# Kernel tuning notes

Hardware: AMD Instinct MI355X
Metric: run time of the kernel (lower is better)

## Reference

```python
import jax, jax.numpy as jnp
import numpy as np

N, E, DIN, H, OUT = 100000, 1600000, 64, 128, 2
BN_EPS = 1e-5


def _mlp_bn(h, wa, ba, g, be, wb, bb):
    # PyG MLP([d_in, H, H]): lin -> batch_norm (train-mode batch stats) -> relu -> lin (plain last)
    h = h @ wa + ba
    mu = jnp.mean(h, axis=0)
    var = jnp.mean((h - mu) ** 2, axis=0)  # biased var, as in BatchNorm training
    h = g * (h - mu) * jax.lax.rsqrt(var + BN_EPS) + be
    h = jax.nn.relu(h)
    return h @ wb + bb


def _gin_layer(x, src, dst, wa, ba, g, be, wb, bb, eps):
    # sum-aggregate neighbor features: agg[i] = sum_{(j->i) in E} x[j]
    agg = jax.ops.segment_sum(x[src], dst, num_segments=N)
    h = (1.0 + eps) * x + agg
    h = _mlp_bn(h, wa, ba, g, be, wb, bb)
    return jax.nn.relu(h)  # GIN.forward outer activation (dropout p=0)


def setup_inputs() -> dict:
    key = jax.random.key(0)
    ks = iter(jax.random.split(key, 40))
    d = {}
    d['x'] = jax.random.normal(next(ks), (N, DIN), dtype=jnp.float32)
    d['edge_index'] = jax.random.randint(next(ks), (2, E), 0, N, dtype=jnp.int64)

    def lin(k, fi, fo):
        return jax.random.normal(k, (fi, fo), dtype=jnp.float32) * (1.0 / np.sqrt(fi))

    fin = DIN
    for l in range(3):
        d[f'w{l}a'] = lin(next(ks), fin, H)
        d[f'b{l}a'] = jnp.zeros((H,), jnp.float32)
        d[f'g{l}'] = jnp.ones((H,), jnp.float32)
        d[f'be{l}'] = jnp.zeros((H,), jnp.float32)
        d[f'w{l}b'] = lin(next(ks), H, H)
        d[f'b{l}b'] = jnp.zeros((H,), jnp.float32)
        d[f'eps{l}'] = jnp.zeros((), jnp.float32)
        fin = H
    d['hwa'] = lin(next(ks), H, H)
    d['hba'] = jnp.zeros((H,), jnp.float32)
    d['hwb'] = lin(next(ks), H, OUT)
    d['hbb'] = jnp.zeros((OUT,), jnp.float32)
    return d


def reference(x, edge_index,
              w0a, b0a, g0, be0, w0b, b0b, eps0,
              w1a, b1a, g1, be1, w1b, b1b, eps1,
              w2a, b2a, g2, be2, w2b, b2b, eps2,
              hwa, hba, hwb, hbb):
    src, dst = edge_index[0], edge_index[1]
    h = _gin_layer(x, src, dst, w0a, b0a, g0, be0, w0b, b0b, eps0)
    h = _gin_layer(h, src, dst, w1a, b1a, g1, be1, w1b, b1b, eps1)
    h = _gin_layer(h, src, dst, w2a, b2a, g2, be2, w2b, b2b, eps2)
    # head MLP([H, H, OUT], norm=None, dropout=0): lin -> relu -> lin
    h = jax.nn.relu(h @ hwa + hba)
    return h @ hwb + hbb
```

## Files before the change

kernel.cpp:

```cpp
#include <hip/hip_runtime.h>

#define NN 100000
#define NE 1600000
#define HD 128
#define NB1 391
#define GG  782

typedef unsigned short u16;
typedef __attribute__((ext_vector_type(8))) short bf16x8;
typedef __attribute__((ext_vector_type(4))) float f32x4;

__device__ __forceinline__ u16 f2b(float f) {
    unsigned u = __builtin_bit_cast(unsigned, f);
    unsigned r = (u + 0x7FFFu + ((u >> 16) & 1u)) >> 16;
    return (u16)r;
}
__device__ __forceinline__ float b2f(u16 h) {
    unsigned u = ((unsigned)h) << 16;
    return __builtin_bit_cast(float, u);
}
__device__ __forceinline__ float lof(unsigned v) {
    return __builtin_bit_cast(float, v << 16);
}
__device__ __forceinline__ float hif(unsigned v) {
    return __builtin_bit_cast(float, v & 0xFFFF0000u);
}
__device__ __forceinline__ unsigned pack2(float a, float b) {
    return (unsigned)f2b(a) | ((unsigned)f2b(b) << 16);
}

__global__ __launch_bounds__(256)
void k_hist(const int* __restrict__ dst, int* __restrict__ degree,
            int* __restrict__ off) {
    int e = blockIdx.x * 256 + threadIdx.x;
    if (e < NE) off[e] = atomicAdd(degree + dst[e], 1);
}

__global__ __launch_bounds__(256)
void k_scan_blk(const int* __restrict__ degree, int* __restrict__ incl,
                int* __restrict__ bsum) {
    __shared__ int s[256];
    int t = threadIdx.x;
    int i = blockIdx.x * 256 + t;
    int v = (i < NN) ? degree[i] : 0;
    s[t] = v;
    __syncthreads();
    #pragma unroll
    for (int off = 1; off < 256; off <<= 1) {
        int tmp = (t >= off) ? s[t - off] : 0;
        __syncthreads();
        s[t] += tmp;
        __syncthreads();
    }
    if (i < NN) incl[i] = s[t];
    if (t == 255) bsum[blockIdx.x] = s[255];
}

__global__ __launch_bounds__(512)
void k_scan_top(const int* __restrict__ bsum, int* __restrict__ bscan) {
    __shared__ int s[512];
    int t = threadIdx.x;
    s[t] = (t < NB1) ? bsum[t] : 0;
    __syncthreads();
    #pragma unroll
    for (int off = 1; off < 512; off <<= 1) {
        int tmp = (t >= off) ? s[t - off] : 0;
        __syncthreads();
        s[t] += tmp;
        __syncthreads();
    }
    if (t < NB1) bscan[t] = s[t];
}

__global__ __launch_bounds__(256)
void k_scan_fix(const int* __restrict__ incl, const int* __restrict__ bscan,
                int* __restrict__ rowptr) {
    int i = blockIdx.x * 256 + threadIdx.x;
    if (i < NN) {
        int off = (blockIdx.x > 0) ? bscan[blockIdx.x - 1] : 0;
        rowptr[i + 1] = incl[i] + off;
        if (i == 0) rowptr[0] = 0;
    }
}

__global__ __launch_bounds__(256)
void k_scatter(const int* __restrict__ src, const int* __restrict__ dst,
               const int* __restrict__ rowptr, const int* __restrict__ off,
               int* __restrict__ eidx) {
    int e = blockIdx.x * 256 + threadIdx.x;
    if (e < NE) {
        eidx[rowptr[dst[e]] + off[e]] = src[e];
    }
}

__global__ __launch_bounds__(256)
void k_cvt(const float* __restrict__ in, u16* __restrict__ out, int n4) {
    for (int i = blockIdx.x * 256 + threadIdx.x; i < n4; i += gridDim.x * 256) {
        float4 v = reinterpret_cast<const float4*>(in)[i];
        uint2 o;
        o.x = pack2(v.x, v.y);
        o.y = pack2(v.z, v.w);
        *reinterpret_cast<uint2*>(out + (size_t)i * 4) = o;
    }
}

template<int F>
__global__ __launch_bounds__(64)
void k_aggr(const u16* __restrict__ x, const int* __restrict__ rowptr,
            const int* __restrict__ eidx, const float* __restrict__ epsp,
            u16* __restrict__ out) {
    const int n = blockIdx.x;
    const int t = threadIdx.x;
    const int p0 = rowptr[n], p1 = rowptr[n + 1];
    const float e1 = 1.0f + epsp[0];

    if constexpr (F == 128) {
        const unsigned off = 2u * t;
        float a0 = 0.f, a1 = 0.f, c0 = 0.f, c1 = 0.f;
        int p = p0;
        for (; p + 3 < p1; p += 4) {
            unsigned v0 = *reinterpret_cast<const unsigned*>(x + (size_t)eidx[p]     * 128 + off);
            unsigned v1 = *reinterpret_cast<const unsigned*>(x + (size_t)eidx[p + 1] * 128 + off);
            unsigned v2 = *reinterpret_cast<const unsigned*>(x + (size_t)eidx[p + 2] * 128 + off);
            unsigned v3 = *reinterpret_cast<const unsigned*>(x + (size_t)eidx[p + 3] * 128 + off);
            a0 += lof(v0); a1 += hif(v0);
            c0 += lof(v1); c1 += hif(v1);
            a0 += lof(v2); a1 += hif(v2);
            c0 += lof(v3); c1 += hif(v3);
        }
        for (; p < p1; ++p) {
            unsigned v0 = *reinterpret_cast<const unsigned*>(x + (size_t)eidx[p] * 128 + off);
            a0 += lof(v0); a1 += hif(v0);
        }
        unsigned xs = *reinterpret_cast<const unsigned*>(x + (size_t)n * 128 + off);
        float o0 = fmaf(e1, lof(xs), a0 + c0);
        float o1 = fmaf(e1, hif(xs), a1 + c1);
        *reinterpret_cast<unsigned*>(out + (size_t)n * 128 + off) = pack2(o0, o1);
    } else {
        float a0 = 0.f, a1 = 0.f;
        int p = p0;
        for (; p + 3 < p1; p += 4) {
            float x0 = b2f(x[(size_t)eidx[p]     * 64 + t]);
            float x1 = b2f(x[(size_t)eidx[p + 1] * 64 + t]);
            float x2 = b2f(x[(size_t)eidx[p + 2] * 64 + t]);
            float x3 = b2f(x[(size_t)eidx[p + 3] * 64 + t]);
            a0 += x0 + x2; a1 += x1 + x3;
        }
        for (; p < p1; ++p) a0 += b2f(x[(size_t)eidx[p] * 64 + t]);
        float xs = b2f(x[(size_t)n * 64 + t]);
        out[(size_t)n * 64 + t] = f2b(fmaf(e1, xs, a0 + a1));
    }
}

template<int K, int PRO, int EPI, int OM, int ABV, int STATS>
__global__ __launch_bounds__(256)
void k_gemm(const void* __restrict__ Av,
            const float* __restrict__ af,
            const float* __restrict__ bff,
            const float* __restrict__ W,
            const float* __restrict__ bias,
            void* __restrict__ Cout,
            float* __restrict__ partial,
            const float* __restrict__ w2,
            const float* __restrict__ b2) {
    __shared__ u16 Whi[128 * K];
    __shared__ u16 Wlo[128 * K];
    __shared__ float redS[4][128];
    __shared__ float redQ[4][128];

    const int t = threadIdx.x;
    const int l = t & 63;
    const int w = t >> 6;
    const int mbase = blockIdx.x * 128 + w * 32;
    const int l15 = l & 15;
    const int lg = l >> 4;

    for (int idx = t; idx < K * 32; idx += 256) {
        int k  = idx >> 5;
        int n0 = (idx & 31) * 4;
        float4 wv = *reinterpret_cast<const float4*>(W + (size_t)k * 128 + n0);
        float wa[4] = {wv.x, wv.y, wv.z, wv.w};
        #pragma unroll
        for (int j = 0; j < 4; ++j) {
            int n = n0 + j;
            int byte = n * (2 * K) + k * 2;
            byte ^= ((n & 7) << 4);
            u16 hi = f2b(wa[j]);
            u16 lo = f2b(wa[j] - b2f(hi));
            *reinterpret_cast<u16*>(reinterpret_cast<char*>(Whi) + byte) = hi;
            *reinterpret_cast<u16*>(reinterpret_cast<char*>(Wlo) + byte) = lo;
        }
    }
    __syncthreads();

    f32x4 acc[2][8];
    #pragma unroll
    for (int i = 0; i < 2; ++i)
        #pragma unroll
        for (int j = 0; j < 8; ++j) acc[i][j] = (f32x4){0.f, 0.f, 0.f, 0.f};

    #pragma unroll
    for (int kc = 0; kc < K / 32; ++kc) {
        bf16x8 whi[8], wlo[8];
        #pragma unroll
        for (int nb = 0; nb < 8; ++nb) {
            int n = nb * 16 + l15;
            int byte = n * (2 * K) + kc * 64 + lg * 16;
            byte ^= ((n & 7) << 4);
            whi[nb] = *reinterpret_cast<const bf16x8*>(
                reinterpret_cast<const char*>(Whi) + byte);
            wlo[nb] = *reinterpret_cast<const bf16x8*>(
                reinterpret_cast<const char*>(Wlo) + byte);
        }
        float aa[8], bb[8];
        if (PRO == 1) {
            int kk = kc * 32 + lg * 8;
            float4 x0 = *reinterpret_cast<const float4*>(af + kk);
            float4 x1 = *reinterpret_cast<const float4*>(af + kk + 4);
            float4 y0 = *reinterpret_cast<const float4*>(bff + kk);
            float4 y1 = *reinterpret_cast<const float4*>(bff + kk + 4);
            aa[0] = x0.x; aa[1] = x0.y; aa[2] = x0.z; aa[3] = x0.w;
            aa[4] = x1.x; aa[5] = x1.y; aa[6] = x1.z; aa[7] = x1.w;
            bb[0] = y0.x; bb[1] = y0.y; bb[2] = y0.z; bb[3] = y0.w;
            bb[4] = y1.x; bb[5] = y1.y; bb[6] = y1.z; bb[7] = y1.w;
        }
        #pragma unroll
        for (int mb = 0; mb < 2; ++mb) {
            int m = mbase + mb * 16 + l15;
            if (ABV == 1) {
                bf16x8 ff = {};
                if (m < NN)
                    ff = *reinterpret_cast<const bf16x8*>(
                        (const u16*)Av + (size_t)m * K + kc * 32 + lg * 8);
                #pragma unroll
                for (int nb = 0; nb < 8; ++nb) {
                    acc[mb][nb] = __builtin_amdgcn_mfma_f32_16x16x32_bf16(
                        whi[nb], ff, acc[mb][nb], 0, 0, 0);
                    acc[mb][nb] = __builtin_amdgcn_mfma_f32_16x16x32_bf16(
                        wlo[nb], ff, acc[mb][nb], 0, 0, 0);
                }
            } else {
                float av[8] = {0.f, 0.f, 0.f, 0.f, 0.f, 0.f, 0.f, 0.f};
                if (m < NN) {
                    const float* ap = (const float*)Av + (size_t)m * K + kc * 32 + lg * 8;
                    float4 x0 = *reinterpret_cast<const float4*>(ap);
                    float4 x1 = *reinterpret_cast<const float4*>(ap + 4);
                    av[0] = x0.x; av[1] = x0.y; av[2] = x0.z; av[3] = x0.w;
                    av[4] = x1.x; av[5] = x1.y; av[6] = x1.z; av[7] = x1.w;
                }
                if (PRO == 1) {
                    #pragma unroll
                    for (int j = 0; j < 8; ++j)
                        av[j] = fmaxf(fmaf(aa[j], av[j], bb[j]), 0.f);
                }
                union { bf16x8 v; u16 s[8]; } uh, ul;
                #pragma unroll
                for (int j = 0; j < 8; ++j) {
                    u16 hi = f2b(av[j]);
                    uh.s[j] = hi;
                    ul.s[j] = f2b(av[j] - b2f(hi));
                }
                #pragma unroll
                for (int nb = 0; nb < 8; ++nb) {
                    acc[mb][nb] = __builtin_amdgcn_mfma_f32_16x16x32_bf16(
                        whi[nb], uh.v, acc[mb][nb], 0, 0, 0);
                    acc[mb][nb] = __builtin_amdgcn_mfma_f32_16x16x32_bf16(
                        whi[nb], ul.v, acc[mb][nb], 0, 0, 0);
                    acc[mb][nb] = __builtin_amdgcn_mfma_f32_16x16x32_bf16(
                        wlo[nb], uh.v, acc[mb][nb], 0, 0, 0);
                }
            }
        }
    }

    if (OM == 2) {
        float o00 = 0.f, o01 = 0.f, o10 = 0.f, o11 = 0.f;
        #pragma unroll
        for (int nb = 0; nb < 8; ++nb) {
            int n0 = nb * 16 + lg * 4;
            float4 b4 = *reinterpret_cast<const float4*>(bias + n0);
            float bv[4] = {b4.x, b4.y, b4.z, b4.w};
            #pragma unroll
            for (int r = 0; r < 4; ++r) {
                int n = n0 + r;
                float w20 = w2[n * 2], w21 = w2[n * 2 + 1];
                float v0 = fmaxf(acc[0][nb][r] + bv[r], 0.f);
                float v1 = fmaxf(acc[1][nb][r] + bv[r], 0.f);
                o00 = fmaf(v0, w20, o00); o01 = fmaf(v0, w21, o01);
                o10 = fmaf(v1, w20, o10); o11 = fmaf(v1, w21, o11);
            }
        }
        o00 += __shfl_xor(o00, 16); o00 += __shfl_xor(o00, 32);
        o01 += __shfl_xor(o01, 16); o01 += __shfl_xor(o01, 32);
        o10 += __shfl_xor(o10, 16); o10 += __shfl_xor(o10, 32);
        o11 += __shfl_xor(o11, 16); o11 += __shfl_xor(o11, 32);
        if (lg == 0) {
            float bb0 = b2[0], bb1 = b2[1];
            float* outp = (float*)Cout;
            int m0 = mbase + l15, m1 = mbase + 16 + l15;
            if (m0 < NN)
                *reinterpret_cast<float2*>(outp + (size_t)m0 * 2) =
                    make_float2(o00 + bb0, o01 + bb1);
            if (m1 < NN)
                *reinterpret_cast<float2*>(outp + (size_t)m1 * 2) =
                    make_float2(o10 + bb0, o11 + bb1);
        }
        return;
    }

    #pragma unroll
    for (int nb = 0; nb < 8; ++nb) {
        int n0 = nb * 16 + lg * 4;
        float4 b4 = *reinterpret_cast<const float4*>(bias + n0);
        float bv[4] = {b4.x, b4.y, b4.z, b4.w};
        float vs[2][4];
        #pragma unroll
        for (int mb = 0; mb < 2; ++mb) {
            int m = mbase + mb * 16 + l15;
            #pragma unroll
            for (int r = 0; r < 4; ++r)
                vs[mb][r] = (m < NN) ? (acc[mb][nb][r] + bv[r]) : 0.f;
        }
        if (STATS == 1) {
            #pragma unroll
            for (int r = 0; r < 4; ++r) {
                float s = vs[0][r] + vs[1][r];
                float q = vs[0][r] * vs[0][r] + vs[1][r] * vs[1][r];
                s += __shfl_xor(s, 1); q += __shfl_xor(q, 1);
                s += __shfl_xor(s, 2); q += __shfl_xor(q, 2);
                s += __shfl_xor(s, 4); q += __shfl_xor(q, 4);
                s += __shfl_xor(s, 8); q += __shfl_xor(q, 8);
                if (l15 == 0) {
                    int n = n0 + r;
                    redS[w][n] = s;
                    redQ[w][n] = q;
                }
            }
        }
        #pragma unroll
        for (int mb = 0; mb < 2; ++mb) {
            int m = mbase + mb * 16 + l15;
            if (m >= NN) continue;
            float v0 = vs[mb][0], v1 = vs[mb][1], v2 = vs[mb][2], v3 = vs[mb][3];
            if (EPI == 1) {
                v0 = fmaxf(v0, 0.f); v1 = fmaxf(v1, 0.f);
                v2 = fmaxf(v2, 0.f); v3 = fmaxf(v3, 0.f);
            }
            if (OM == 1) {
                uint2 o;
                o.x = pack2(v0, v1);
                o.y = pack2(v2, v3);
                *reinterpret_cast<uint2*>((u16*)Cout + (size_t)m * 128 + n0) = o;
            } else {
                float4 o = make_float4(v0, v1, v2, v3);
                *reinterpret_cast<float4*>((float*)Cout + (size_t)m * 128 + n0) = o;
            }
        }
    }

    if (STATS == 1) {
        __syncthreads();
        if (t < 128) {
            float s = redS[0][t] + redS[1][t] + redS[2][t] + redS[3][t];
            float q = redQ[0][t] + redQ[1][t] + redQ[2][t] + redQ[3][t];
            partial[(size_t)blockIdx.x * 256 + t] = s;
            partial[(size_t)blockIdx.x * 256 + 128 + t] = q;
        }
    }
}

__global__ __launch_bounds__(256)
void k_bnfin2(const float* __restrict__ partial,
              const float* __restrict__ g, const float* __restrict__ be,
              float* __restrict__ af, float* __restrict__ bf) {
    const int c = blockIdx.x;
    const int t = threadIdx.x;
    __shared__ double sS[256];
    __shared__ double sQ[256];
    double S = 0.0, Q = 0.0;
    for (int b = t; b < GG; b += 256) {
        S += (double)partial[(size_t)b * 256 + c];
        Q += (double)partial[(size_t)b * 256 + 128 + c];
    }
    sS[t] = S; sQ[t] = Q;
    __syncthreads();
    #pragma unroll
    for (int off = 128; off > 0; off >>= 1) {
        if (t < off) { sS[t] += sS[t + off]; sQ[t] += sQ[t + off]; }
        __syncthreads();
    }
    if (t == 0) {
        double mu  = sS[0] / (double)NN;
        double var = sQ[0] / (double)NN - mu * mu;
        double a   = (double)g[c] / sqrt(var + 1e-5);
        af[c] = (float)a;
        bf[c] = be[c] - (float)(mu * a);
    }
}

extern "C" void kernel_launch(void* const* d_in, const int* in_sizes, int n_in,
                              void* d_out, int out_size, void* d_ws, size_t ws_size,
                              hipStream_t stream) {
    const float* x  = (const float*)d_in[0];
    const int*   ei = (const int*)d_in[1];
    const int* src = ei;
    const int* dst = ei + NE;
    auto P = [&](int i) { return (const float*)d_in[i]; };

    const size_t BUFF = (size_t)NN * HD * sizeof(float);
    const size_t BUFH = (size_t)NN * HD * sizeof(u16);
    char* ws = (char*)d_ws;
    u16*   gB   = (u16*)(ws);
    u16*   aggB = (u16*)(ws + BUFH);
    float* yF   = (float*)(ws + 2 * BUFH);
    float* hF   = (float*)(ws + 2 * BUFH + BUFF);
    u16*   xb   = (u16*)(ws + 2 * BUFH + 2 * BUFF);
    char*  sb   = ws + 2 * BUFH + 2 * BUFF + (size_t)NN * 64 * sizeof(u16);
    float* partial = (float*)sb;
    float* af = (float*)(sb + (size_t)GG * 256 * 4);
    float* bf = af + 128;
    int* degree = (int*)(af + 256);
    int* incl   = degree + NN;
    int* bsum   = incl + NN;
    int* bscan  = bsum + 512;
    int* rowptr = bscan + 512;
    int* eoff   = rowptr + NN + 2;
    int* eidx   = eoff + NE;

    const int EGRID = (NE + 255) / 256;

    hipMemsetAsync(degree, 0, NN * sizeof(int), stream);
    k_hist<<<EGRID, 256, 0, stream>>>(dst, degree, eoff);
    k_scan_blk<<<NB1, 256, 0, stream>>>(degree, incl, bsum);
    k_scan_top<<<1, 512, 0, stream>>>(bsum, bscan);
    k_scan_fix<<<NB1, 256, 0, stream>>>(incl, bscan, rowptr);
    k_scatter<<<EGRID, 256, 0, stream>>>(src, dst, rowptr, eoff, eidx);

    k_cvt<<<2048, 256, 0, stream>>>(x, xb, NN * 64 / 4);

    k_aggr<64><<<NN, 64, 0, stream>>>(xb, rowptr, eidx, P(8), aggB);
    k_gemm<64, 0, 0, 0, 1, 1><<<GG, 256, 0, stream>>>(
        aggB, nullptr, nullptr, P(2), P(3), yF, partial, nullptr, nullptr);
    k_bnfin2<<<128, 256, 0, stream>>>(partial, P(4), P(5), af, bf);
    k_gemm<128, 1, 1, 1, 0, 0><<<GG, 256, 0, stream>>>(
        yF, af, bf, P(6), P(7), gB, nullptr, nullptr, nullptr);

    k_aggr<128><<<NN, 64, 0, stream>>>(gB, rowptr, eidx, P(15), aggB);
    k_gemm<128, 0, 0, 0, 1, 1><<<GG, 256, 0, stream>>>(
        aggB, nullptr, nullptr, P(9), P(10), yF, partial, nullptr, nullptr);
    k_bnfin2<<<128, 256, 0, stream>>>(partial, P(11), P(12), af, bf);
    k_gemm<128, 1, 1, 1, 0, 0><<<GG, 256, 0, stream>>>(
        yF, af, bf, P(13), P(14), gB, nullptr, nullptr, nullptr);

    k_aggr<128><<<NN, 64, 0, stream>>>(gB, rowptr, eidx, P(22), aggB);
    k_gemm<128, 0, 0, 0, 1, 1><<<GG, 256, 0, stream>>>(
        aggB, nullptr, nullptr, P(16), P(17), yF, partial, nullptr, nullptr);
    k_bnfin2<<<128, 256, 0, stream>>>(partial, P(18), P(19), af, bf);
    k_gemm<128, 1, 1, 0, 0, 0><<<GG, 256, 0, stream>>>(
        yF, af, bf, P(20), P(21), hF, nullptr, nullptr, nullptr);

    k_gemm<128, 0, 1, 2, 0, 0><<<GG, 256, 0, stream>>>(
        hF, nullptr, nullptr, P(23), P(24), (float*)d_out, nullptr, P(25), P(26));
}
```

Measured before the change: 735.8 us.

## Build CSR via two-level bucket sort with shared-memory atomics

Replaces the global-atomic histogram, three-pass scan and random scatter CSR build with a bucketed counting sort. Edges are first binned into 391 buckets of 256 destination nodes using shared-memory counters, then each bucket is finalized in its own block with a local histogram, scan and placement. The aim is fewer contended global atomics and more localized writes, at the cost of an extra pairs buffer and an extra pass over the edges.

```diff
diff --git a/kernel.cpp b/kernel.cpp
--- a/kernel.cpp
+++ b/kernel.cpp
@@ -3,8 +3,9 @@
 #define NN 100000
 #define NE 1600000
 #define HD 128
-#define NB1 391
 #define GG  782
+#define NBKT 391
+#define BW_SH 8
 
 typedef unsigned short u16;
 typedef __attribute__((ext_vector_type(8))) short bf16x8;
@@ -30,37 +31,29 @@
 }
 
 __global__ __launch_bounds__(256)
-void k_hist(const int* __restrict__ dst, int* __restrict__ degree,
-            int* __restrict__ off) {
-    int e = blockIdx.x * 256 + threadIdx.x;
-    if (e < NE) off[e] = atomicAdd(degree + dst[e], 1);
-}
-
-__global__ __launch_bounds__(256)
-void k_scan_blk(const int* __restrict__ degree, int* __restrict__ incl,
-                int* __restrict__ bsum) {
-    __shared__ int s[256];
-    int t = threadIdx.x;
-    int i = blockIdx.x * 256 + t;
-    int v = (i < NN) ? degree[i] : 0;
+void k_bcount(const int* __restrict__ dst, int* __restrict__ bucketCnt) {
+    __shared__ int cnt[NBKT];
+    const int t = threadIdx.x;
+    for (int i = t; i < NBKT; i += 256) cnt[i] = 0;
+    __syncthreads();
+    int e0 = blockIdx.x * 4096 + t;
+    #pragma unroll
+    for (int i = 0; i < 16; ++i) {
+        int e = e0 + i * 256;
+        if (e < NE) atomicAdd(&cnt[dst[e] >> BW_SH], 1);
+    }
+    __syncthreads();
+    for (int i = t; i < NBKT; i += 256)
+        if (cnt[i]) atomicAdd(bucketCnt + i, cnt[i]);
+}
+
+__global__ __launch_bounds__(512)
+void k_bscan(const int* __restrict__ bucketCnt, int* __restrict__ bucketBase,
+             int* __restrict__ bucketCur) {
+    __shared__ int s[512];
+    const int t = threadIdx.x;
+    int v = (t < NBKT) ? bucketCnt[t] : 0;
     s[t] = v;
-    __syncthreads();
-    #pragma unroll
-    for (int off = 1; off < 256; off <<= 1) {
-        int tmp = (t >= off) ? s[t - off] : 0;
-        __syncthreads();
-        s[t] += tmp;
-        __syncthreads();
-    }
-    if (i < NN) incl[i] = s[t];
-    if (t == 255) bsum[blockIdx.x] = s[255];
-}
-
-__global__ __launch_bounds__(512)
-void k_scan_top(const int* __restrict__ bsum, int* __restrict__ bscan) {
-    __shared__ int s[512];
-    int t = threadIdx.x;
-    s[t] = (t < NB1) ? bsum[t] : 0;
     __syncthreads();
     #pragma unroll
     for (int off = 1; off < 512; off <<= 1) {
@@ -69,27 +62,77 @@
         s[t] += tmp;
         __syncthreads();
     }
-    if (t < NB1) bscan[t] = s[t];
+    if (t < NBKT) {
+        bucketBase[t + 1] = s[t];
+        bucketCur[t] = s[t] - v;
+        if (t == 0) bucketBase[0] = 0;
+    }
 }
 
 __global__ __launch_bounds__(256)
-void k_scan_fix(const int* __restrict__ incl, const int* __restrict__ bscan,
-                int* __restrict__ rowptr) {
-    int i = blockIdx.x * 256 + threadIdx.x;
-    if (i < NN) {
-        int off = (blockIdx.x > 0) ? bscan[blockIdx.x - 1] : 0;
-        rowptr[i + 1] = incl[i] + off;
-        if (i == 0) rowptr[0] = 0;
+void k_bscatter(const int* __restrict__ src, const int* __restrict__ dst,
+                int* __restrict__ bucketCur, int2* __restrict__ pairs) {
+    __shared__ int cnt[NBKT];
+    __shared__ int cbase[NBKT];
+    const int t = threadIdx.x;
+    for (int i = t; i < NBKT; i += 256) cnt[i] = 0;
+    __syncthreads();
+    int e0 = blockIdx.x * 4096 + t;
+    int db[16];
+    #pragma unroll
+    for (int i = 0; i < 16; ++i) {
+        int e = e0 + i * 256;
+        db[i] = (e < NE) ? dst[e] : -1;
+        if (db[i] >= 0) atomicAdd(&cnt[db[i] >> BW_SH], 1);
+    }
+    __syncthreads();
+    for (int i = t; i < NBKT; i += 256)
+        cbase[i] = cnt[i] ? atomicAdd(bucketCur + i, cnt[i]) : 0;
+    __syncthreads();
+    for (int i = t; i < NBKT; i += 256) cnt[i] = 0;
+    __syncthreads();
+    #pragma unroll
+    for (int i = 0; i < 16; ++i) {
+        int e = e0 + i * 256;
+        if (e < NE) {
+            int b = db[i] >> BW_SH;
+            int r = atomicAdd(&cnt[b], 1);
+            pairs[cbase[b] + r] = make_int2(src[e], db[i]);
+        }
     }
 }
 
 __global__ __launch_bounds__(256)
-void k_scatter(const int* __restrict__ src, const int* __restrict__ dst,
-               const int* __restrict__ rowptr, const int* __restrict__ off,
-               int* __restrict__ eidx) {
-    int e = blockIdx.x * 256 + threadIdx.x;
-    if (e < NE) {
-        eidx[rowptr[dst[e]] + off[e]] = src[e];
+void k_bfinal(const int2* __restrict__ pairs, const int* __restrict__ bucketBase,
+              int* __restrict__ rowptr, int* __restrict__ eidx) {
+    __shared__ int deg[256], pfx[256], cur[256];
+    const int b = blockIdx.x, t = threadIdx.x;
+    const int n0 = b << BW_SH;
+    const int bb = bucketBase[b], be = bucketBase[b + 1];
+    deg[t] = 0;
+    __syncthreads();
+    for (int e = bb + t; e < be; e += 256)
+        atomicAdd(&deg[pairs[e].y & 255], 1);
+    __syncthreads();
+    int v = deg[t];
+    pfx[t] = v;
+    __syncthreads();
+    #pragma unroll
+    for (int off = 1; off < 256; off <<= 1) {
+        int tmp = (t >= off) ? pfx[t - off] : 0;
+        __syncthreads();
+        pfx[t] += tmp;
+        __syncthreads();
+    }
+    int n = n0 + t;
+    if (n < NN) rowptr[n + 1] = bb + pfx[t];
+    if (b == 0 && t == 0) rowptr[0] = 0;
+    cur[t] = bb + pfx[t] - v;
+    __syncthreads();
+    for (int e = bb + t; e < be; e += 256) {
+        int2 p = pairs[e];
+        int pos = atomicAdd(&cur[p.y & 255], 1);
+        eidx[pos] = p.x;
     }
 }
 
@@ -419,22 +462,20 @@
     float* partial = (float*)sb;
     float* af = (float*)(sb + (size_t)GG * 256 * 4);
     float* bf = af + 128;
-    int* degree = (int*)(af + 256);
-    int* incl   = degree + NN;
-    int* bsum   = incl + NN;
-    int* bscan  = bsum + 512;
-    int* rowptr = bscan + 512;
-    int* eoff   = rowptr + NN + 2;
-    int* eidx   = eoff + NE;
-
-    const int EGRID = (NE + 255) / 256;
-
-    hipMemsetAsync(degree, 0, NN * sizeof(int), stream);
-    k_hist<<<EGRID, 256, 0, stream>>>(dst, degree, eoff);
-    k_scan_blk<<<NB1, 256, 0, stream>>>(degree, incl, bsum);
-    k_scan_top<<<1, 512, 0, stream>>>(bsum, bscan);
-    k_scan_fix<<<NB1, 256, 0, stream>>>(incl, bscan, rowptr);
-    k_scatter<<<EGRID, 256, 0, stream>>>(src, dst, rowptr, eoff, eidx);
+    int* bucketCnt  = (int*)(af + 256);
+    int* bucketBase = bucketCnt + NBKT + 1;
+    int* bucketCur  = bucketBase + NBKT + 1;
+    int* rowptr     = bucketCur + NBKT + 1;
+    int* eidx       = rowptr + NN + 3;
+    int2* pairs     = (int2*)(((size_t)(eidx + NE) + 15) & ~(size_t)15);
+
+    const int EBLK = (NE + 4095) / 4096;
+
+    hipMemsetAsync(bucketCnt, 0, NBKT * sizeof(int), stream);
+    k_bcount<<<EBLK, 256, 0, stream>>>(dst, bucketCnt);
+    k_bscan<<<1, 512, 0, stream>>>(bucketCnt, bucketBase, bucketCur);
+    k_bscatter<<<EBLK, 256, 0, stream>>>(src, dst, bucketCur, pairs);
+    k_bfinal<<<NBKT, 256, 0, stream>>>(pairs, bucketBase, rowptr, eidx);
 
     k_cvt<<<2048, 256, 0, stream>>>(x, xb, NN * 64 / 4);
 
```

Measured after the change: 711.9 us. -3.2%, faster.
